# Optimization experiments

Hardware: AMD Instinct MI355X
Metric: run time of the kernel (lower is better)

The kernel has to match this reference:

```python
import jax, jax.numpy as jnp
import numpy as np

N = 50000
E = 600000
IN1, IN2, HID, OUT = 256, 128, 128, 64


def gcn_conv(x, W, b, src, dst, n):
    """PyG GCNConv: D^{-1/2}(A+I)D^{-1/2} X W + b with self-loops."""
    h = x @ W  # [N, F_out]
    # degree including self-loop (edge weight 1)
    deg = jax.ops.segment_sum(jnp.ones_like(dst, dtype=h.dtype), dst, num_segments=n) + 1.0
    dinv = deg ** -0.5
    coef = dinv[src] * dinv[dst]  # [E]
    agg = jax.ops.segment_sum(h[src] * coef[:, None], dst, num_segments=n)
    agg = agg + h * (dinv * dinv)[:, None]  # self-loop contribution
    return agg + b


def gcn_stack(x, edge_index, Ws, bs, n):
    src, dst = edge_index[0], edge_index[1]
    x = jax.nn.relu(gcn_conv(x, Ws[0], bs[0], src, dst, n))
    return gcn_conv(x, Ws[1], bs[1], src, dst, n)


def setup_inputs() -> dict:
    key = jax.random.key(0)
    ks = jax.random.split(key, 12)
    glorot = lambda k, fi, fo: jax.random.normal(k, (fi, fo), jnp.float32) * np.sqrt(2.0 / (fi + fo))
    return {
        "x1": jax.random.normal(ks[0], (N, IN1), jnp.float32),
        "edge_index1": jax.random.randint(ks[1], (2, E), 0, N, jnp.int32),
        "x2": jax.random.normal(ks[2], (N, IN2), jnp.float32),
        "edge_index2": jax.random.randint(ks[3], (2, E), 0, N, jnp.int32),
        "W1_0": glorot(ks[4], IN1, HID), "b1_0": jnp.zeros((HID,), jnp.float32),
        "W1_1": glorot(ks[5], HID, OUT), "b1_1": jnp.zeros((OUT,), jnp.float32),
        "W2_0": glorot(ks[6], IN2, HID), "b2_0": jnp.zeros((HID,), jnp.float32),
        "W2_1": glorot(ks[7], HID, OUT), "b2_1": jnp.zeros((OUT,), jnp.float32),
    }


def reference(x1, edge_index1, x2, edge_index2,
              W1_0, b1_0, W1_1, b1_1, W2_0, b2_0, W2_1, b2_1):
    out1 = gcn_stack(x1, edge_index1, (W1_0, W1_1), (b1_0, b1_1), N)
    out2 = gcn_stack(x2, edge_index2, (W2_0, W2_1), (b2_0, b2_1), N)
    return out1, out2
```

## Files before the change

kernel.cpp:

```cpp
#include <hip/hip_runtime.h>
#include <hip/hip_bf16.h>
#include <cstdint>
#include <type_traits>

static constexpr int NN = 50000;
static constexpr int NE = 600000;
static constexpr int NB = (NN + 255) / 256;
static constexpr int CHUNK = 1024;
static constexpr int NCH = (NE + CHUNK - 1) / CHUNK;
static constexpr int CAP = 4096;

typedef __bf16 bf16;
typedef __attribute__((ext_vector_type(2))) __bf16 bf16x2;
typedef __attribute__((ext_vector_type(8))) __bf16 bf16x8;
typedef __attribute__((ext_vector_type(4))) float f32x4;

__global__ __launch_bounds__(256) void k_init(int* __restrict__ bucketcur,
                                              int* __restrict__ row_off) {
    int i = blockIdx.x * 256 + threadIdx.x;
    if (i < 2 * NB) bucketcur[i] = i * CAP;
    if (i < 2) row_off[i * (NN + 1) + NN] = NE;
}

__global__ __launch_bounds__(256) void k_binA(const int* __restrict__ srcA,
                                              const int* __restrict__ dstA,
                                              const int* __restrict__ srcB,
                                              const int* __restrict__ dstB,
                                              int* __restrict__ bucketcur,
                                              int2* __restrict__ stg) {
    __shared__ int cnt[NB];
    __shared__ int ibase[NB];
    int g = blockIdx.y;
    const int* src = g ? srcB : srcA;
    const int* dst = g ? dstB : dstA;
    int tid = threadIdx.x;
    int c0 = blockIdx.x * CHUNK;
    if (tid < NB) cnt[tid] = 0;
    __syncthreads();
    #pragma unroll
    for (int it = 0; it < CHUNK / 256; ++it) {
        int e = c0 + it * 256 + tid;
        if (e < NE) atomicAdd(&cnt[dst[e] >> 8], 1);
    }
    __syncthreads();
    if (tid < NB) {
        int c = cnt[tid];
        ibase[tid] = c ? atomicAdd(&bucketcur[g * NB + tid], c) : 0;
        cnt[tid] = 0;
    }
    __syncthreads();
    #pragma unroll
    for (int it = 0; it < CHUNK / 256; ++it) {
        int e = c0 + it * 256 + tid;
        if (e < NE) {
            int s = src[e], d = dst[e];
            int b = d >> 8;
            int p = atomicAdd(&cnt[b], 1);
            stg[(size_t)ibase[b] + p] = make_int2(s, d);
        }
    }
}

__global__ __launch_bounds__(256) void k_bucket_scan(const int* __restrict__ bucketcur,
                                                     int* __restrict__ bucket_base) {
    __shared__ int s[256];
    int g = blockIdx.x;
    int tid = threadIdx.x;
    int B = g * NB + tid;
    int v = (tid < NB) ? bucketcur[B] - B * CAP : 0;
    s[tid] = v;
    __syncthreads();
    for (int off = 1; off < 256; off <<= 1) {
        int t = (tid >= off) ? s[tid - off] : 0;
        __syncthreads();
        s[tid] += t;
        __syncthreads();
    }
    if (tid < NB) bucket_base[B] = s[tid] - v;
}

__global__ __launch_bounds__(256) void k_binB1(const int2* __restrict__ stg,
                                               const int* __restrict__ bucketcur,
                                               const int* __restrict__ bucket_base,
                                               int* __restrict__ row_off,
                                               float* __restrict__ dinv) {
    __shared__ int cnt[256];
    __shared__ int s[256];
    int g = blockIdx.y;
    int b = blockIdx.x;
    int B = g * NB + b;
    int tid = threadIdx.x;
    int node0 = b << 8;
    int nnod = min(256, NN - node0);
    cnt[tid] = 0;
    __syncthreads();
    int count = bucketcur[B] - B * CAP;
    const int2* s0 = stg + (size_t)B * CAP;
    for (int j = tid; j < count; j += 256)
        atomicAdd(&cnt[s0[j].y - node0], 1);
    __syncthreads();
    int v = cnt[tid];
    s[tid] = v;
    __syncthreads();
    for (int off = 1; off < 256; off <<= 1) {
        int t = (tid >= off) ? s[tid - off] : 0;
        __syncthreads();
        s[tid] += t;
        __syncthreads();
    }
    if (tid < nnod) {
        row_off[g * (NN + 1) + node0 + tid] = bucket_base[B] + s[tid] - v;
        dinv[(size_t)g * NN + node0 + tid] = rsqrtf((float)v + 1.0f);
    }
}

__global__ __launch_bounds__(256) void k_binB2(const int2* __restrict__ stg,
                                               const int* __restrict__ bucketcur,
                                               const int* __restrict__ row_off,
                                               const float* __restrict__ dinv,
                                               int2* __restrict__ pair) {
    __shared__ int lcur[256];
    __shared__ float ldv[256];
    int g = blockIdx.y;
    int b = blockIdx.x;
    int B = g * NB + b;
    int tid = threadIdx.x;
    int node0 = b << 8;
    int nnod = min(256, NN - node0);
    const int* ro = row_off + g * (NN + 1);
    if (tid < nnod) {
        lcur[tid] = ro[node0 + tid];
        ldv[tid] = dinv[(size_t)g * NN + node0 + tid];
    }
    __syncthreads();
    int count = bucketcur[B] - B * CAP;
    const int2* s0 = stg + (size_t)B * CAP;
    for (int j = tid; j < count; j += 256) {
        int2 sd = s0[j];
        int rel = sd.y - node0;
        int pos = atomicAdd(&lcur[rel], 1);
        float cf = dinv[(size_t)g * NN + sd.x] * ldv[rel];
        pair[(size_t)g * NE + pos] = make_int2(sd.x, __float_as_int(cf));
    }
}

__global__ __launch_bounds__(256) void k_wprep4(const float* __restrict__ WA,
                                                const float* __restrict__ WB,
                                                const float* __restrict__ WC,
                                                const float* __restrict__ WD,
                                                bf16* __restrict__ wf0,
                                                bf16* __restrict__ wf1) {
    int y = blockIdx.y;
    const float* W = (y == 0) ? WA : (y == 1) ? WB : (y == 2) ? WC : WD;
    bf16* wf = (y == 0) ? wf0 : (y == 1) ? wf0 + 256 * 128 : (y == 2) ? wf1 : wf1 + 128 * 64;
    int K = (y == 0) ? 256 : 128;
    int F = (y <= 1) ? 128 : 64;
    int i = blockIdx.x * 256 + threadIdx.x;
    if (i < K * F) {
        int k = i / F, n = i % F;
        wf[((size_t)(k >> 3) * F + n) * 8 + (k & 7)] = (bf16)W[i];
    }
}

template <int K, int F, typename AT>
__device__ __forceinline__ void gemm_body(const AT* __restrict__ X,
                                          const bf16* __restrict__ wf,
                                          bf16* __restrict__ H, int n, int bx) {
    constexpr int NT = F / 16;
    int wave = threadIdx.x >> 6;
    int lane = threadIdx.x & 63;
    int lm = lane & 15;
    int lk = lane >> 4;
    int r0 = bx * 64 + wave * 16;

    int arow = r0 + lm;
    if (arow >= n) arow = n - 1;
    const AT* xrow = X + (size_t)arow * K;

    f32x4 acc[NT] = {};

    for (int k0 = 0; k0 < K; k0 += 32) {
        bf16x8 af;
        if constexpr (std::is_same_v<AT, float>) {
            f32x4 a0 = *reinterpret_cast<const f32x4*>(xrow + k0 + lk * 8);
            f32x4 a1 = *reinterpret_cast<const f32x4*>(xrow + k0 + lk * 8 + 4);
            af[0] = (bf16)a0.x; af[1] = (bf16)a0.y; af[2] = (bf16)a0.z; af[3] = (bf16)a0.w;
            af[4] = (bf16)a1.x; af[5] = (bf16)a1.y; af[6] = (bf16)a1.z; af[7] = (bf16)a1.w;
        } else {
            af = *reinterpret_cast<const bf16x8*>(xrow + k0 + lk * 8);
        }
        const bf16* wbase = wf + ((size_t)(k0 / 8 + lk) * F) * 8;
        #pragma unroll
        for (int t = 0; t < NT; ++t) {
            bf16x8 bfg = *reinterpret_cast<const bf16x8*>(wbase + (t * 16 + lm) * 8);
            acc[t] = __builtin_amdgcn_mfma_f32_16x16x32_bf16(af, bfg, acc[t], 0, 0, 0);
        }
    }

    #pragma unroll
    for (int t = 0; t < NT; ++t) {
        #pragma unroll
        for (int i = 0; i < 4; ++i) {
            int gr = r0 + lk * 4 + i;
            if (gr < n) H[(size_t)gr * F + t * 16 + lm] = (bf16)acc[t][i];
        }
    }
}

static constexpr int GB = (NN + 63) / 64;

__global__ __launch_bounds__(256) void gemm_l1(const float* __restrict__ x1,
                                               const float* __restrict__ x2,
                                               const bf16* __restrict__ wf0,
                                               bf16* __restrict__ h) {
    int bx = blockIdx.x;
    if (bx < GB)
        gemm_body<256, 128, float>(x1, wf0, h, NN, bx);
    else
        gemm_body<128, 128, float>(x2, wf0 + 256 * 128, h + (size_t)NN * 128, NN, bx - GB);
}

__global__ __launch_bounds__(256) void gemm_l2(const bf16* __restrict__ a,
                                               const bf16* __restrict__ wf1,
                                               bf16* __restrict__ h2) {
    int bx = blockIdx.x;
    int g = (bx >= GB);
    gemm_body<128, 64, bf16>(a + (size_t)g * NN * 128, wf1 + g * 128 * 64,
                             h2 + (size_t)g * NN * 64, NN, bx - g * GB);
}

__global__ __launch_bounds__(256) void agg128_2(const bf16* __restrict__ hb,
                                                const int* __restrict__ row_off,
                                                const int2* __restrict__ pairb,
                                                const float* __restrict__ dinv,
                                                const float* __restrict__ biasA,
                                                const float* __restrict__ biasB,
                                                bf16* __restrict__ ab) {
    int wid = blockIdx.x * 4 + (threadIdx.x >> 6);
    if (wid >= 2 * NN) return;
    int g = (wid >= NN);
    int node = wid - g * NN;
    int lane = threadIdx.x & 63;

    const bf16* h = hb + (size_t)g * NN * 128;
    const int2* pair = pairb + (size_t)g * NE;
    const int* ro = row_off + g * (NN + 1);
    const float* bias = g ? biasB : biasA;

    int f = lane * 2;
    float di = dinv[g * NN + node];
    int beg = ro[node];
    int end = ro[node + 1];

    float a0 = 0.f, a1 = 0.f;

    auto edge1 = [&](int2 p) {
        float c = __int_as_float(p.y);
        bf16x2 v = *reinterpret_cast<const bf16x2*>(&h[(size_t)p.x * 128 + f]);
        a0 = fmaf((float)v[0], c, a0); a1 = fmaf((float)v[1], c, a1);
    };
    auto edge2 = [&](int4 q) {
        float cA = __int_as_float(q.y), cB = __int_as_float(q.w);
        bf16x2 vA = *reinterpret_cast<const bf16x2*>(&h[(size_t)q.x * 128 + f]);
        bf16x2 vB = *reinterpret_cast<const bf16x2*>(&h[(size_t)q.z * 128 + f]);
        a0 = fmaf((float)vA[0], cA, a0); a1 = fmaf((float)vA[1], cA, a1);
        a0 = fmaf((float)vB[0], cB, a0); a1 = fmaf((float)vB[1], cB, a1);
    };

    int j = beg;
    if ((j & 1) && j < end) { edge1(pair[j]); ++j; }
    for (; j + 7 < end; j += 8) {
        int4 q0 = *reinterpret_cast<const int4*>(&pair[j]);
        int4 q1 = *reinterpret_cast<const int4*>(&pair[j + 2]);
        int4 q2 = *reinterpret_cast<const int4*>(&pair[j + 4]);
        int4 q3 = *reinterpret_cast<const int4*>(&pair[j + 6]);
        edge2(q0); edge2(q1); edge2(q2); edge2(q3);
    }
    for (; j + 1 < end; j += 2) {
        int4 q = *reinterpret_cast<const int4*>(&pair[j]);
        edge2(q);
    }
    if (j < end) edge1(pair[j]);

    bf16x2 hv = *reinterpret_cast<const bf16x2*>(&h[(size_t)node * 128 + f]);
    float sc = di * di;
    a0 = fmaf((float)hv[0], sc, a0) + bias[f];
    a1 = fmaf((float)hv[1], sc, a1) + bias[f + 1];
    a0 = fmaxf(a0, 0.f);
    a1 = fmaxf(a1, 0.f);

    bf16x2 r;
    r[0] = (bf16)a0; r[1] = (bf16)a1;
    *reinterpret_cast<bf16x2*>(&ab[((size_t)g * NN + node) * 128 + f]) = r;
}

__global__ __launch_bounds__(256) void agg64_2(const bf16* __restrict__ h2b,
                                               const int* __restrict__ row_off,
                                               const int2* __restrict__ pairb,
                                               const float* __restrict__ dinv,
                                               const float* __restrict__ biasA,
                                               const float* __restrict__ biasB,
                                               float* __restrict__ outb) {
    int wid = blockIdx.x * 4 + (threadIdx.x >> 6);
    if (wid >= 2 * NN) return;
    int g = (wid >= NN);
    int node = wid - g * NN;
    int lane = threadIdx.x & 63;

    const bf16* h = h2b + (size_t)g * NN * 64;
    const int2* pair = pairb + (size_t)g * NE;
    const int* ro = row_off + g * (NN + 1);
    const float* bias = g ? biasB : biasA;
    float* out = outb + (size_t)g * NN * 64;

    int half = lane >> 5;
    int f = (lane & 31) * 2;
    float di = dinv[(size_t)g * NN + node];
    int beg = ro[node];
    int end = ro[node + 1];

    float a0 = 0.f, a1 = 0.f;

    auto edge = [&](int2 p) {
        float c = __int_as_float(p.y);
        bf16x2 v = *reinterpret_cast<const bf16x2*>(&h[(size_t)p.x * 64 + f]);
        a0 = fmaf((float)v[0], c, a0); a1 = fmaf((float)v[1], c, a1);
    };

    int j = beg;
    for (; j + 7 < end; j += 8) {
        int2 p0 = pair[j + half], p1 = pair[j + 2 + half];
        int2 p2 = pair[j + 4 + half], p3 = pair[j + 6 + half];
        edge(p0); edge(p1); edge(p2); edge(p3);
    }
    for (; j + 1 < end; j += 2) edge(pair[j + half]);
    if (j < end && half == 0) edge(pair[j]);

    a0 += __shfl_xor(a0, 32);
    a1 += __shfl_xor(a1, 32);

    bf16x2 hv = *reinterpret_cast<const bf16x2*>(&h[(size_t)node * 64 + f]);
    float sc = di * di;
    a0 = fmaf((float)hv[0], sc, a0) + bias[f];
    a1 = fmaf((float)hv[1], sc, a1) + bias[f + 1];

    if (half == 0) {
        out[(size_t)node * 64 + f] = a0;
        out[(size_t)node * 64 + f + 1] = a1;
    }
}

extern "C" void kernel_launch(void* const* d_in, const int* in_sizes, int n_in,
                              void* d_out, int out_size, void* d_ws, size_t ws_size,
                              hipStream_t stream) {
    const float* x1 = (const float*)d_in[0];
    const int* ei1 = (const int*)d_in[1];
    const float* x2 = (const float*)d_in[2];
    const int* ei2 = (const int*)d_in[3];
    const float* W1_0 = (const float*)d_in[4];
    const float* b1_0 = (const float*)d_in[5];
    const float* W1_1 = (const float*)d_in[6];
    const float* b1_1 = (const float*)d_in[7];
    const float* W2_0 = (const float*)d_in[8];
    const float* b2_0 = (const float*)d_in[9];
    const float* W2_1 = (const float*)d_in[10];
    const float* b2_1 = (const float*)d_in[11];

    float* out = (float*)d_out;

    char* ws = (char*)d_ws;
    size_t off = 0;
    auto alloc = [&](size_t bytes) {
        size_t o = off;
        off = (off + bytes + 255) & ~(size_t)255;
        return o;
    };
    bf16* h = (bf16*)(ws + alloc((size_t)2 * NN * 128 * 2));
    size_t r2 = (size_t)2 * NB * CAP * 8;
    char* region2 = ws + alloc(r2);
    int2* stg = (int2*)region2;
    bf16* h2 = (bf16*)region2;
    bf16* a = (bf16*)(ws + alloc((size_t)2 * NN * 128 * 2));
    int2* pair = (int2*)(ws + alloc((size_t)2 * NE * 8));
    int* row_off = (int*)(ws + alloc((size_t)2 * (NN + 1) * 4));
    float* dinv = (float*)(ws + alloc((size_t)2 * NN * 4));
    int* bucketcur = (int*)(ws + alloc((size_t)2 * NB * 4));
    int* bucket_base = (int*)(ws + alloc((size_t)2 * NB * 4));
    bf16* wf0 = (bf16*)(ws + alloc((size_t)2 * 256 * 128 * 2));
    bf16* wf1 = (bf16*)(ws + alloc((size_t)2 * 128 * 64 * 2));

    const int* srcA = ei1, *dstA = ei1 + NE;
    const int* srcB = ei2, *dstB = ei2 + NE;

    k_init<<<(2 * NB + 255) / 256, 256, 0, stream>>>(bucketcur, row_off);
    k_wprep4<<<dim3(128, 4), 256, 0, stream>>>(W1_0, W2_0, W1_1, W2_1, wf0, wf1);
    k_binA<<<dim3(NCH, 2), 256, 0, stream>>>(srcA, dstA, srcB, dstB, bucketcur, stg);
    k_bucket_scan<<<2, 256, 0, stream>>>(bucketcur, bucket_base);
    k_binB1<<<dim3(NB, 2), 256, 0, stream>>>(stg, bucketcur, bucket_base, row_off, dinv);
    k_binB2<<<dim3(NB, 2), 256, 0, stream>>>(stg, bucketcur, row_off, dinv, pair);

    gemm_l1<<<2 * GB, 256, 0, stream>>>(x1, x2, wf0, h);
    agg128_2<<<(2 * NN + 3) / 4, 256, 0, stream>>>(h, row_off, pair, dinv, b1_0, b2_0, a);
    gemm_l2<<<2 * GB, 256, 0, stream>>>(a, wf1, h2);
    agg64_2<<<(2 * NN + 3) / 4, 256, 0, stream>>>(h2, row_off, pair, dinv, b1_1, b2_1, out);
}
```

Before: 201.7 us.

## Merge layer-1 GEMM with edge binning and fold init and bucket scan into neighbors

Folds the init kernel into the weight-prep kernel as an extra grid row. It also merges the layer-1 GEMM and the edge-binning pass into a single launch with block-range dispatch, so the compute-bound GEMM and the atomic-heavy binning can overlap on the GPU. The separate bucket-scan kernel is removed and each binB1 block redoes the small 196-entry prefix scan itself. The aim is to cut four launches and the serialization gaps between them. The cost is some redundant scan work per block and shared-memory arrays allocated but unused in GEMM blocks, which may lower occupancy.

```diff
diff --git a/kernel.cpp b/kernel.cpp
--- a/kernel.cpp
+++ b/kernel.cpp
@@ -15,14 +15,83 @@
 typedef __attribute__((ext_vector_type(8))) __bf16 bf16x8;
 typedef __attribute__((ext_vector_type(4))) float f32x4;
 
-__global__ __launch_bounds__(256) void k_init(int* __restrict__ bucketcur,
-                                              int* __restrict__ row_off) {
+__global__ __launch_bounds__(256) void k_wprep4(const float* __restrict__ WA,
+                                                const float* __restrict__ WB,
+                                                const float* __restrict__ WC,
+                                                const float* __restrict__ WD,
+                                                bf16* __restrict__ wf0,
+                                                bf16* __restrict__ wf1,
+                                                int* __restrict__ bucketcur,
+                                                int* __restrict__ row_off) {
+    int y = blockIdx.y;
     int i = blockIdx.x * 256 + threadIdx.x;
-    if (i < 2 * NB) bucketcur[i] = i * CAP;
-    if (i < 2) row_off[i * (NN + 1) + NN] = NE;
-}
-
-__global__ __launch_bounds__(256) void k_binA(const int* __restrict__ srcA,
+    if (y == 4) {
+        if (i < 2 * NB) bucketcur[i] = i * CAP;
+        if (i < 2) row_off[i * (NN + 1) + NN] = NE;
+        return;
+    }
+    const float* W = (y == 0) ? WA : (y == 1) ? WB : (y == 2) ? WC : WD;
+    bf16* wf = (y == 0) ? wf0 : (y == 1) ? wf0 + 256 * 128 : (y == 2) ? wf1 : wf1 + 128 * 64;
+    int K = (y == 0) ? 256 : 128;
+    int F = (y <= 1) ? 128 : 64;
+    if (i < K * F) {
+        int k = i / F, n = i % F;
+        wf[((size_t)(k >> 3) * F + n) * 8 + (k & 7)] = (bf16)W[i];
+    }
+}
+
+template <int K, int F, typename AT>
+__device__ __forceinline__ void gemm_body(const AT* __restrict__ X,
+                                          const bf16* __restrict__ wf,
+                                          bf16* __restrict__ H, int n, int bx) {
+    constexpr int NT = F / 16;
+    int wave = threadIdx.x >> 6;
+    int lane = threadIdx.x & 63;
+    int lm = lane & 15;
+    int lk = lane >> 4;
+    int r0 = bx * 64 + wave * 16;
+
+    int arow = r0 + lm;
+    if (arow >= n) arow = n - 1;
+    const AT* xrow = X + (size_t)arow * K;
+
+    f32x4 acc[NT] = {};
+
+    for (int k0 = 0; k0 < K; k0 += 32) {
+        bf16x8 af;
+        if constexpr (std::is_same_v<AT, float>) {
+            f32x4 a0 = *reinterpret_cast<const f32x4*>(xrow + k0 + lk * 8);
+            f32x4 a1 = *reinterpret_cast<const f32x4*>(xrow + k0 + lk * 8 + 4);
+            af[0] = (bf16)a0.x; af[1] = (bf16)a0.y; af[2] = (bf16)a0.z; af[3] = (bf16)a0.w;
+            af[4] = (bf16)a1.x; af[5] = (bf16)a1.y; af[6] = (bf16)a1.z; af[7] = (bf16)a1.w;
+        } else {
+            af = *reinterpret_cast<const bf16x8*>(xrow + k0 + lk * 8);
+        }
+        const bf16* wbase = wf + ((size_t)(k0 / 8 + lk) * F) * 8;
+        #pragma unroll
+        for (int t = 0; t < NT; ++t) {
+            bf16x8 bfg = *reinterpret_cast<const bf16x8*>(wbase + (t * 16 + lm) * 8);
+            acc[t] = __builtin_amdgcn_mfma_f32_16x16x32_bf16(af, bfg, acc[t], 0, 0, 0);
+        }
+    }
+
+    #pragma unroll
+    for (int t = 0; t < NT; ++t) {
+        #pragma unroll
+        for (int i = 0; i < 4; ++i) {
+            int gr = r0 + lk * 4 + i;
+            if (gr < n) H[(size_t)gr * F + t * 16 + lm] = (bf16)acc[t][i];
+        }
+    }
+}
+
+static constexpr int GB = (NN + 63) / 64;
+
+__global__ __launch_bounds__(256) void k_mega(const float* __restrict__ x1,
+                                              const float* __restrict__ x2,
+                                              const bf16* __restrict__ wf0,
+                                              bf16* __restrict__ h,
+                                              const int* __restrict__ srcA,
                                               const int* __restrict__ dstA,
                                               const int* __restrict__ srcB,
                                               const int* __restrict__ dstB,
@@ -30,11 +99,21 @@
                                               int2* __restrict__ stg) {
     __shared__ int cnt[NB];
     __shared__ int ibase[NB];
-    int g = blockIdx.y;
+    int bx = blockIdx.x;
+    if (bx < 2 * GB) {
+        if (bx < GB)
+            gemm_body<256, 128, float>(x1, wf0, h, NN, bx);
+        else
+            gemm_body<128, 128, float>(x2, wf0 + 256 * 128, h + (size_t)NN * 128, NN, bx - GB);
+        return;
+    }
+    int cx = bx - 2 * GB;
+    int g = (cx >= NCH);
+    int chunk = cx - g * NCH;
     const int* src = g ? srcB : srcA;
     const int* dst = g ? dstB : dstA;
     int tid = threadIdx.x;
-    int c0 = blockIdx.x * CHUNK;
+    int c0 = chunk * CHUNK;
     if (tid < NB) cnt[tid] = 0;
     __syncthreads();
     #pragma unroll
@@ -61,14 +140,20 @@
     }
 }
 
-__global__ __launch_bounds__(256) void k_bucket_scan(const int* __restrict__ bucketcur,
-                                                     int* __restrict__ bucket_base) {
+__global__ __launch_bounds__(256) void k_binB1(const int2* __restrict__ stg,
+                                               const int* __restrict__ bucketcur,
+                                               int* __restrict__ row_off,
+                                               float* __restrict__ dinv) {
+    __shared__ int cnt[256];
     __shared__ int s[256];
-    int g = blockIdx.x;
+    __shared__ int bb[256];
+    int g = blockIdx.y;
+    int b = blockIdx.x;
+    int B = g * NB + b;
     int tid = threadIdx.x;
-    int B = g * NB + tid;
-    int v = (tid < NB) ? bucketcur[B] - B * CAP : 0;
-    s[tid] = v;
+
+    int cv = (tid < NB) ? bucketcur[g * NB + tid] - (g * NB + tid) * CAP : 0;
+    s[tid] = cv;
     __syncthreads();
     for (int off = 1; off < 256; off <<= 1) {
         int t = (tid >= off) ? s[tid - off] : 0;
@@ -76,24 +161,13 @@
         s[tid] += t;
         __syncthreads();
     }
-    if (tid < NB) bucket_base[B] = s[tid] - v;
-}
-
-__global__ __launch_bounds__(256) void k_binB1(const int2* __restrict__ stg,
-                                               const int* __restrict__ bucketcur,
-                                               const int* __restrict__ bucket_base,
-                                               int* __restrict__ row_off,
-                                               float* __restrict__ dinv) {
-    __shared__ int cnt[256];
-    __shared__ int s[256];
-    int g = blockIdx.y;
-    int b = blockIdx.x;
-    int B = g * NB + b;
-    int tid = threadIdx.x;
+    if (tid < NB) bb[tid] = s[tid] - cv;
+    cnt[tid] = 0;
+    __syncthreads();
+    int base = bb[b];
+
     int node0 = b << 8;
     int nnod = min(256, NN - node0);
-    cnt[tid] = 0;
-    __syncthreads();
     int count = bucketcur[B] - B * CAP;
     const int2* s0 = stg + (size_t)B * CAP;
     for (int j = tid; j < count; j += 256)
@@ -109,7 +183,7 @@
         __syncthreads();
     }
     if (tid < nnod) {
-        row_off[g * (NN + 1) + node0 + tid] = bucket_base[B] + s[tid] - v;
+        row_off[g * (NN + 1) + node0 + tid] = base + s[tid] - v;
         dinv[(size_t)g * NN + node0 + tid] = rsqrtf((float)v + 1.0f);
     }
 }
@@ -144,82 +218,6 @@
     }
 }
 
-__global__ __launch_bounds__(256) void k_wprep4(const float* __restrict__ WA,
-                                                const float* __restrict__ WB,
-                                                const float* __restrict__ WC,
-                                                const float* __restrict__ WD,
-                                                bf16* __restrict__ wf0,
-                                                bf16* __restrict__ wf1) {
-    int y = blockIdx.y;
-    const float* W = (y == 0) ? WA : (y == 1) ? WB : (y == 2) ? WC : WD;
-    bf16* wf = (y == 0) ? wf0 : (y == 1) ? wf0 + 256 * 128 : (y == 2) ? wf1 : wf1 + 128 * 64;
-    int K = (y == 0) ? 256 : 128;
-    int F = (y <= 1) ? 128 : 64;
-    int i = blockIdx.x * 256 + threadIdx.x;
-    if (i < K * F) {
-        int k = i / F, n = i % F;
-        wf[((size_t)(k >> 3) * F + n) * 8 + (k & 7)] = (bf16)W[i];
-    }
-}
-
-template <int K, int F, typename AT>
-__device__ __forceinline__ void gemm_body(const AT* __restrict__ X,
-                                          const bf16* __restrict__ wf,
-                                          bf16* __restrict__ H, int n, int bx) {
-    constexpr int NT = F / 16;
-    int wave = threadIdx.x >> 6;
-    int lane = threadIdx.x & 63;
-    int lm = lane & 15;
-    int lk = lane >> 4;
-    int r0 = bx * 64 + wave * 16;
-
-    int arow = r0 + lm;
-    if (arow >= n) arow = n - 1;
-    const AT* xrow = X + (size_t)arow * K;
-
-    f32x4 acc[NT] = {};
-
-    for (int k0 = 0; k0 < K; k0 += 32) {
-        bf16x8 af;
-        if constexpr (std::is_same_v<AT, float>) {
-            f32x4 a0 = *reinterpret_cast<const f32x4*>(xrow + k0 + lk * 8);
-            f32x4 a1 = *reinterpret_cast<const f32x4*>(xrow + k0 + lk * 8 + 4);
-            af[0] = (bf16)a0.x; af[1] = (bf16)a0.y; af[2] = (bf16)a0.z; af[3] = (bf16)a0.w;
-            af[4] = (bf16)a1.x; af[5] = (bf16)a1.y; af[6] = (bf16)a1.z; af[7] = (bf16)a1.w;
-        } else {
-            af = *reinterpret_cast<const bf16x8*>(xrow + k0 + lk * 8);
-        }
-        const bf16* wbase = wf + ((size_t)(k0 / 8 + lk) * F) * 8;
-        #pragma unroll
-        for (int t = 0; t < NT; ++t) {
-            bf16x8 bfg = *reinterpret_cast<const bf16x8*>(wbase + (t * 16 + lm) * 8);
-            acc[t] = __builtin_amdgcn_mfma_f32_16x16x32_bf16(af, bfg, acc[t], 0, 0, 0);
-        }
-    }
-
-    #pragma unroll
-    for (int t = 0; t < NT; ++t) {
-        #pragma unroll
-        for (int i = 0; i < 4; ++i) {
-            int gr = r0 + lk * 4 + i;
-            if (gr < n) H[(size_t)gr * F + t * 16 + lm] = (bf16)acc[t][i];
-        }
-    }
-}
-
-static constexpr int GB = (NN + 63) / 64;
-
-__global__ __launch_bounds__(256) void gemm_l1(const float* __restrict__ x1,
-                                               const float* __restrict__ x2,
-                                               const bf16* __restrict__ wf0,
-                                               bf16* __restrict__ h) {
-    int bx = blockIdx.x;
-    if (bx < GB)
-        gemm_body<256, 128, float>(x1, wf0, h, NN, bx);
-    else
-        gemm_body<128, 128, float>(x2, wf0 + 256 * 128, h + (size_t)NN * 128, NN, bx - GB);
-}
-
 __global__ __launch_bounds__(256) void gemm_l2(const bf16* __restrict__ a,
                                                const bf16* __restrict__ wf1,
                                                bf16* __restrict__ h2) {
@@ -385,21 +383,19 @@
     int* row_off = (int*)(ws + alloc((size_t)2 * (NN + 1) * 4));
     float* dinv = (float*)(ws + alloc((size_t)2 * NN * 4));
     int* bucketcur = (int*)(ws + alloc((size_t)2 * NB * 4));
-    int* bucket_base = (int*)(ws + alloc((size_t)2 * NB * 4));
     bf16* wf0 = (bf16*)(ws + alloc((size_t)2 * 256 * 128 * 2));
     bf16* wf1 = (bf16*)(ws + alloc((size_t)2 * 128 * 64 * 2));
 
     const int* srcA = ei1, *dstA = ei1 + NE;
     const int* srcB = ei2, *dstB = ei2 + NE;
 
-    k_init<<<(2 * NB + 255) / 256, 256, 0, stream>>>(bucketcur, row_off);
-    k_wprep4<<<dim3(128, 4), 256, 0, stream>>>(W1_0, W2_0, W1_1, W2_1, wf0, wf1);
-    k_binA<<<dim3(NCH, 2), 256, 0, stream>>>(srcA, dstA, srcB, dstB, bucketcur, stg);
-    k_bucket_scan<<<2, 256, 0, stream>>>(bucketcur, bucket_base);
-    k_binB1<<<dim3(NB, 2), 256, 0, stream>>>(stg, bucketcur, bucket_base, row_off, dinv);
+    k_wprep4<<<dim3(128, 5), 256, 0, stream>>>(W1_0, W2_0, W1_1, W2_1, wf0, wf1,
+                                               bucketcur, row_off);
+    k_mega<<<2 * GB + 2 * NCH, 256, 0, stream>>>(x1, x2, wf0, h,
+                                                 srcA, dstA, srcB, dstB, bucketcur, stg);
+    k_binB1<<<dim3(NB, 2), 256, 0, stream>>>(stg, bucketcur, row_off, dinv);
     k_binB2<<<dim3(NB, 2), 256, 0, stream>>>(stg, bucketcur, row_off, dinv, pair);
 
-    gemm_l1<<<2 * GB, 256, 0, stream>>>(x1, x2, wf0, h);
     agg128_2<<<(2 * NN + 3) / 4, 256, 0, stream>>>(h, row_off, pair, dinv, b1_0, b2_0, a);
     gemm_l2<<<2 * GB, 256, 0, stream>>>(a, wf1, h2);
     agg64_2<<<(2 * NN + 3) / 4, 256, 0, stream>>>(h2, row_off, pair, dinv, b1_1, b2_1, out);
```

After: 193.0 us. 1.05x faster.
